# Kernel optimization log

Measured on AMD Instinct MI355X. Metric: run time of the kernel, lower is better.

## Reference

```python
import jax, jax.numpy as jnp
import numpy as np
import math

DIM = 1024
N_HEADS = 16
HEAD_DIM = DIM // N_HEADS
MAX_SEQ_LEN = 2048


def rope_tables(seq_len, head_dim):
    inv_freq = 1.0 / (10000.0 ** (jnp.arange(0, head_dim, 2, dtype=jnp.float32) / head_dim))
    t = jnp.arange(seq_len, dtype=jnp.float32)
    freqs = jnp.einsum('i,j->ij', t, inv_freq)          # [T, D/2]
    emb = jnp.concatenate([freqs, freqs], axis=-1)      # [T, D]
    return jnp.cos(emb), jnp.sin(emb)


def rotate_half(x):
    x1, x2 = jnp.split(x, 2, axis=-1)
    return jnp.concatenate([-x2, x1], axis=-1)


def setup_inputs() -> dict:
    key = jax.random.key(0)
    k1, k2, k3 = jax.random.split(key, 3)
    B, T = 4, 2048
    x = jax.random.normal(k1, (B, T, DIM), dtype=jnp.float32)
    # Linear(dim, 3*dim, bias=False) and Linear(dim, dim, bias=False); stored as [in, out]
    Wqkv = jax.random.normal(k2, (DIM, 3 * DIM), dtype=jnp.float32) * (1.0 / math.sqrt(DIM))
    Wproj = jax.random.normal(k3, (DIM, DIM), dtype=jnp.float32) * (1.0 / math.sqrt(DIM))
    return {"x": x, "Wqkv": Wqkv, "Wproj": Wproj}


def reference(x, Wqkv, Wproj):
    B, T, C = x.shape
    qkv = x @ Wqkv                                       # [B,T,3C]
    q, k, v = jnp.split(qkv, 3, axis=-1)
    # [B,T,C] -> [B,H,T,D]
    def to_heads(t_):
        return t_.reshape(B, T, N_HEADS, HEAD_DIM).transpose(0, 2, 1, 3)
    q, k, v = to_heads(q), to_heads(k), to_heads(v)
    cos, sin = rope_tables(T, HEAD_DIM)                  # [T,D]
    cos = cos[None, None, :, :]
    sin = sin[None, None, :, :]
    q = q * cos + rotate_half(q) * sin
    k = k * cos + rotate_half(k) * sin
    scale = 1.0 / math.sqrt(HEAD_DIM)
    att = jnp.einsum('bhqd,bhkd->bhqk', q, k) * scale    # [B,H,T,T]
    causal = jnp.triu(jnp.ones((T, T), dtype=bool), k=1)
    att = jnp.where(causal[None, None], -jnp.inf, att)
    att = jax.nn.softmax(att, axis=-1)
    y = jnp.einsum('bhqk,bhkd->bhqd', att, v)            # [B,H,T,D]
    y = y.transpose(0, 2, 1, 3).reshape(B, T, C)
    return y @ Wproj
```

## Files before the change

### kernel.cpp

```cpp
#include <hip/hip_runtime.h>
#include <hip/hip_bf16.h>

typedef unsigned short u16;
typedef __attribute__((ext_vector_type(8))) short short8;
typedef __attribute__((ext_vector_type(4))) float floatx4;

__device__ __forceinline__ u16 f2bf(float f) {
    union { float f; unsigned u; } v; v.f = f;
    unsigned r = v.u + 0x7fffu + ((v.u >> 16) & 1u);
    return (u16)(r >> 16);
}
__device__ __forceinline__ float fexp2(float x) {
#if __has_builtin(__builtin_amdgcn_exp2f)
    return __builtin_amdgcn_exp2f(x);
#else
    return exp2f(x);
#endif
}

__device__ __forceinline__ void async_load16(const void* g, void* l) {
    __builtin_amdgcn_global_load_lds(
        (const __attribute__((address_space(1))) unsigned int*)g,
        (__attribute__((address_space(3))) unsigned int*)l, 16, 0, 0);
}

#define B_   4
#define T_   2048
#define NH_  16
#define HD_  64
#define DIM_ 1024
#define M_   (B_ * T_)
#define NQKV (3 * DIM_)
#define LOG2E 1.4426950408889634f

__global__ void cvt_x(const float* __restrict__ in, u16* __restrict__ out) {
    int idx = blockIdx.x * 256 + threadIdx.x;
    float4 v = ((const float4*)in)[idx];
    ushort4 o;
    o.x = f2bf(v.x); o.y = f2bf(v.y); o.z = f2bf(v.z); o.w = f2bf(v.w);
    ((ushort4*)out)[idx] = o;
}

__global__ void transpose_cvt(const float* __restrict__ in, u16* __restrict__ out,
                              int R, int Cn) {
    __shared__ float tile[32][33];
    int c0 = blockIdx.x * 32, r0 = blockIdx.y * 32;
    int tx = threadIdx.x, ty = threadIdx.y;
#pragma unroll
    for (int i = 0; i < 4; ++i)
        tile[ty + i * 8][tx] = in[(size_t)(r0 + ty + i * 8) * Cn + c0 + tx];
    __syncthreads();
#pragma unroll
    for (int i = 0; i < 4; ++i)
        out[(size_t)(c0 + ty + i * 8) * R + r0 + tx] = f2bf(tile[tx][ty + i * 8]);
}

__global__ void rope_table(float* __restrict__ tabc, float* __restrict__ tabs) {
    int idx = blockIdx.x * 256 + threadIdx.x;
    if (idx >= T_ * 32) return;
    int t = idx >> 5, j = idx & 31;
    double invf = pow(10000.0, -(double)j / 32.0);
    double th = (double)t * invf;
    tabc[idx] = (float)cos(th);
    tabs[idx] = (float)sin(th);
}

__global__ void v_transpose(const u16* __restrict__ Vh, u16* __restrict__ Vt) {
    __shared__ u16 tile[64 * 68];
    const int tid = threadIdx.x;
    const int bh = blockIdx.y, b = bh >> 4, h = bh & 15;
    const int t0 = blockIdx.x * 64;
    {
        int lr = tid >> 2;
        int lc = tid & 3;
        const u16* src = Vh + ((size_t)(b * T_ + t0 + lr)) * DIM_ + h * HD_;
#pragma unroll
        for (int j = 0; j < 4; ++j) {
            int c = (lc + j * 4) * 4;
            *(uint2*)&tile[lr * 68 + c] = *(const uint2*)(src + c);
        }
    }
    __syncthreads();
    {
        int d2 = tid >> 3, tseg = tid & 7;
        u16 lo8[8], hi8[8];
#pragma unroll
        for (int j = 0; j < 8; ++j) {
            unsigned w = *(const unsigned*)&tile[(tseg * 8 + j) * 68 + d2 * 2];
            lo8[j] = (u16)(w & 0xffffu);
            hi8[j] = (u16)(w >> 16);
        }
        size_t ob = ((size_t)bh * HD_ + 2 * d2) * T_ + t0 + tseg * 8;
        *(uint4*)(Vt + ob) = *(const uint4*)lo8;
        *(uint4*)(Vt + ob + T_) = *(const uint4*)hi8;
    }
}

__global__ __launch_bounds__(256) void gemm_qkv(const u16* __restrict__ A,
                                                const u16* __restrict__ Bt,
                                                const float* __restrict__ tabc,
                                                const float* __restrict__ tabs,
                                                u16* __restrict__ Qo,
                                                u16* __restrict__ Ko,
                                                u16* __restrict__ Vh) {
    __shared__ __align__(16) u16 smem[2 * 128 * 64];
    u16* Asl = smem;
    u16* Bsl = smem + 128 * 64;
    const int tid = threadIdx.x;
    const int wave = tid >> 6, lane = tid & 63;
    const int ln15 = lane & 15, quad = lane >> 4;
    const int m0 = blockIdx.y * 128, n0 = blockIdx.x * 128;
    const int wm = (wave & 1) * 64, wn = (wave >> 1) * 64;
    const int l8 = lane & 7, ld8 = lane >> 3;
    const int sgc = (l8 ^ ld8) * 8;
    const int K = DIM_;

    floatx4 acc[4][4] = {};

    for (int k0 = 0; k0 < K; k0 += 64) {
#pragma unroll
        for (int it = 0; it < 4; ++it) {
            int rb = wave * 32 + it * 8;
            async_load16(A  + (size_t)(m0 + rb + ld8) * K + k0 + sgc, &Asl[rb * 64]);
            async_load16(Bt + (size_t)(n0 + rb + ld8) * K + k0 + sgc, &Bsl[rb * 64]);
        }
        __syncthreads();
#pragma unroll
        for (int kk = 0; kk < 64; kk += 32) {
            const int c4 = kk >> 3;
            short8 af[4], bfm[4];
#pragma unroll
            for (int i = 0; i < 4; ++i) {
                int row = wm + i * 16 + ln15;
                af[i] = *(const short8*)&Asl[row * 64 + (((c4 + quad) ^ (row & 7)) << 3)];
            }
#pragma unroll
            for (int jj = 0; jj < 4; ++jj) {
                int row = wn + jj * 16 + ln15;
                bfm[jj] = *(const short8*)&Bsl[row * 64 + (((c4 + quad) ^ (row & 7)) << 3)];
            }
#pragma unroll
            for (int i = 0; i < 4; ++i)
#pragma unroll
                for (int jj = 0; jj < 4; ++jj)
                    acc[i][jj] = __builtin_amdgcn_mfma_f32_16x16x32_bf16(
                        af[i], bfm[jj], acc[i][jj], 0, 0, 0);
        }
        __syncthreads();
    }

    u16* Es = smem;
    const int sel = n0 >> 10;
    auto es_put = [&](int row, int col, u16 v) {
        int c = col >> 3;
        int pc = (c & 8) | ((c & 7) ^ (row & 7));
        Es[row * 128 + pc * 8 + (col & 7)] = v;
    };
    if (sel == 2) {
#pragma unroll
        for (int i = 0; i < 4; ++i)
#pragma unroll
            for (int jj = 0; jj < 4; ++jj)
#pragma unroll
                for (int r = 0; r < 4; ++r)
                    es_put(wm + i * 16 + quad * 4 + r, wn + jj * 16 + ln15,
                           f2bf(acc[i][jj][r]));
    } else {
        const float scale = sel ? 1.0f : 0.125f * LOG2E;
#pragma unroll
        for (int i = 0; i < 4; ++i)
#pragma unroll
            for (int jjl = 0; jjl < 2; ++jjl) {
                int j = jjl * 16 + ln15;
#pragma unroll
                for (int r = 0; r < 4; ++r) {
                    int row = wm + i * 16 + quad * 4 + r;
                    int t = (m0 + row) & (T_ - 1);
                    float cs = tabc[t * 32 + j], sn = tabs[t * 32 + j];
                    float xl = acc[i][jjl][r], xh = acc[i][jjl + 2][r];
                    es_put(row, wn + j,      f2bf((xl * cs - xh * sn) * scale));
                    es_put(row, wn + j + 32, f2bf((xh * cs + xl * sn) * scale));
                }
            }
    }
    __syncthreads();
    const int bb = m0 >> 11;
    u16* outqk = (sel == 1) ? Ko : Qo;
#pragma unroll
    for (int k = 0; k < 8; ++k) {
        int cid = tid + k * 256;
        int row = cid >> 4, c = cid & 15;
        int pc = (c & 8) | ((c & 7) ^ (row & 7));
        uint4 v = *(const uint4*)&Es[row * 128 + pc * 8];
        if (sel == 2) {
            *(uint4*)&Vh[(size_t)(m0 + row) * DIM_ + (n0 & 1023) + c * 8] = v;
        } else {
            int h = ((n0 & 1023) >> 6) + (c >> 3);
            int d = (c & 7) * 8;
            int t = (m0 + row) & (T_ - 1);
            *(uint4*)&outqk[((size_t)(bb * NH_ + h) * T_ + t) * HD_ + d] = v;
        }
    }
}

__global__ __launch_bounds__(256) void gemm_bt_f32(const u16* __restrict__ A,
                                                   const u16* __restrict__ Bt,
                                                   float* __restrict__ C,
                                                   int M, int N, int K) {
    __shared__ __align__(16) u16 Asl[128 * 64];
    __shared__ __align__(16) u16 Bsl[128 * 64];
    const int tid = threadIdx.x;
    const int wave = tid >> 6, lane = tid & 63;
    const int ln15 = lane & 15, quad = lane >> 4;
    const int m0 = blockIdx.y * 128, n0 = blockIdx.x * 128;
    const int wm = (wave & 1) * 64, wn = (wave >> 1) * 64;
    const int l8 = lane & 7, ld8 = lane >> 3;
    const int sgc = (l8 ^ ld8) * 8;

    floatx4 acc[4][4] = {};

    for (int k0 = 0; k0 < K; k0 += 64) {
#pragma unroll
        for (int it = 0; it < 4; ++it) {
            int rb = wave * 32 + it * 8;
            async_load16(A  + (size_t)(m0 + rb + ld8) * K + k0 + sgc, &Asl[rb * 64]);
            async_load16(Bt + (size_t)(n0 + rb + ld8) * K + k0 + sgc, &Bsl[rb * 64]);
        }
        __syncthreads();
#pragma unroll
        for (int kk = 0; kk < 64; kk += 32) {
            const int c4 = kk >> 3;
            short8 af[4], bfm[4];
#pragma unroll
            for (int i = 0; i < 4; ++i) {
                int row = wm + i * 16 + ln15;
                af[i] = *(const short8*)&Asl[row * 64 + (((c4 + quad) ^ (row & 7)) << 3)];
            }
#pragma unroll
            for (int jj = 0; jj < 4; ++jj) {
                int row = wn + jj * 16 + ln15;
                bfm[jj] = *(const short8*)&Bsl[row * 64 + (((c4 + quad) ^ (row & 7)) << 3)];
            }
#pragma unroll
            for (int i = 0; i < 4; ++i)
#pragma unroll
                for (int jj = 0; jj < 4; ++jj)
                    acc[i][jj] = __builtin_amdgcn_mfma_f32_16x16x32_bf16(
                        af[i], bfm[jj], acc[i][jj], 0, 0, 0);
        }
        __syncthreads();
    }
#pragma unroll
    for (int i = 0; i < 4; ++i)
#pragma unroll
        for (int jj = 0; jj < 4; ++jj)
#pragma unroll
            for (int r = 0; r < 4; ++r) {
                int m = m0 + wm + i * 16 + quad * 4 + r;
                int n = n0 + wn + jj * 16 + ln15;
                C[(size_t)m * N + n] = acc[i][jj][r];
            }
}

__global__ __launch_bounds__(256, 4) void attn_kernel(const u16* __restrict__ Q,
                                                      const u16* __restrict__ Kh,
                                                      const u16* __restrict__ Vt,
                                                      u16* __restrict__ Y) {
    __shared__ __align__(16) u16 Kl[2][64 * 64];
    __shared__ __align__(16) u16 Vl[2][64 * 64];
    __shared__ __align__(16) u16 Pl[4][16 * 64];
    const int tid = threadIdx.x, wave = tid >> 6, lane = tid & 63;
    const int ln15 = lane & 15, quad = lane >> 4;
    const int p = blockIdx.x;
    const int bh = blockIdx.y;
    const int b = bh >> 4, h = bh & 15;
    const int l8 = lane & 7, ld8 = lane >> 3;
    const int sgc = l8 ^ ld8;

    const u16* kbase = Kh + (size_t)bh * T_ * HD_;
    const u16* vbase = Vt + (size_t)bh * HD_ * T_;
    const short8 ones = {0x3F80, 0x3F80, 0x3F80, 0x3F80,
                         0x3F80, 0x3F80, 0x3F80, 0x3F80};
    const int srow = wave * 16;

#pragma unroll
    for (int half = 0; half < 2; ++half) {
        const int tidx = half ? p : (31 - p);
        const int q0 = tidx * 64;
        const int bm = q0 + srow;

        const u16* qp = Q + ((size_t)bh * T_ + bm + ln15) * HD_;
        short8 qf0 = *(const short8*)(qp + quad * 8);
        short8 qf1 = *(const short8*)(qp + 32 + quad * 8);

        floatx4 o[5] = {};

        __syncthreads();
#pragma unroll
        for (int it = 0; it < 2; ++it) {
            int r = srow + it * 8;
            async_load16(kbase + (size_t)(r + ld8) * HD_ + sgc * 8, &Kl[0][r * 64]);
            async_load16(vbase + (size_t)(r + ld8) * T_ + sgc * 8, &Vl[0][r * 64]);
        }

        for (int kt = 0; kt <= tidx; ++kt) {
            const int cur = kt & 1;
            __syncthreads();
            if (kt < tidx) {
                const int kn = (kt + 1) * 64;
#pragma unroll
                for (int it = 0; it < 2; ++it) {
                    int r = srow + it * 8;
                    async_load16(kbase + (size_t)(kn + r + ld8) * HD_ + sgc * 8,
                                 &Kl[cur ^ 1][r * 64]);
                    async_load16(vbase + (size_t)(r + ld8) * T_ + kn + sgc * 8,
                                 &Vl[cur ^ 1][r * 64]);
                }
            }
            floatx4 s[4] = {};
#pragma unroll
            for (int nt = 0; nt < 4; ++nt) {
                int row = nt * 16 + ln15;
                short8 kf0 = *(const short8*)&Kl[cur][row * 64 + ((quad ^ (row & 7)) << 3)];
                short8 kf1 = *(const short8*)&Kl[cur][row * 64 + (((4 + quad) ^ (row & 7)) << 3)];
                s[nt] = __builtin_amdgcn_mfma_f32_16x16x32_bf16(qf0, kf0, s[nt], 0, 0, 0);
                s[nt] = __builtin_amdgcn_mfma_f32_16x16x32_bf16(qf1, kf1, s[nt], 0, 0, 0);
            }
            if (kt == tidx) {
#pragma unroll
                for (int nt = 0; nt < 4; ++nt) {
                    int key = nt * 16 + ln15, lim = srow + quad * 4;
#pragma unroll
                    for (int r = 0; r < 4; ++r)
                        s[nt][r] = (key > lim + r) ? 0.f : fexp2(s[nt][r]);
                }
            } else {
#pragma unroll
                for (int nt = 0; nt < 4; ++nt)
#pragma unroll
                    for (int r = 0; r < 4; ++r) s[nt][r] = fexp2(s[nt][r]);
            }
            u16* pw = Pl[wave];
#pragma unroll
            for (int nt = 0; nt < 4; ++nt) {
                int kc = nt * 2 + (ln15 >> 3), k7 = ln15 & 7;
#pragma unroll
                for (int r = 0; r < 4; ++r) {
                    int row = quad * 4 + r;
                    pw[row * 64 + ((kc ^ (row & 7)) << 3) + k7] = f2bf(s[nt][r]);
                }
            }
            short8 pf0 = *(const short8*)&pw[ln15 * 64 + ((quad ^ (ln15 & 7)) << 3)];
            short8 pf1 = *(const short8*)&pw[ln15 * 64 + (((4 + quad) ^ (ln15 & 7)) << 3)];
#pragma unroll
            for (int nt = 0; nt < 4; ++nt) {
                int row = nt * 16 + ln15;
                short8 vf0 = *(const short8*)&Vl[cur][row * 64 + ((quad ^ (row & 7)) << 3)];
                short8 vf1 = *(const short8*)&Vl[cur][row * 64 + (((4 + quad) ^ (row & 7)) << 3)];
                o[nt] = __builtin_amdgcn_mfma_f32_16x16x32_bf16(pf0, vf0, o[nt], 0, 0, 0);
                o[nt] = __builtin_amdgcn_mfma_f32_16x16x32_bf16(pf1, vf1, o[nt], 0, 0, 0);
            }
            o[4] = __builtin_amdgcn_mfma_f32_16x16x32_bf16(pf0, ones, o[4], 0, 0, 0);
            o[4] = __builtin_amdgcn_mfma_f32_16x16x32_bf16(pf1, ones, o[4], 0, 0, 0);
        }
#pragma unroll
        for (int r = 0; r < 4; ++r) {
            float inv = 1.f / o[4][r];
            int row = bm + quad * 4 + r;
            u16* yp = Y + ((size_t)(b * T_ + row)) * DIM_ + h * HD_;
#pragma unroll
            for (int nt = 0; nt < 4; ++nt)
                yp[nt * 16 + ln15] = f2bf(o[nt][r] * inv);
        }
    }
}

extern "C" void kernel_launch(void* const* d_in, const int* in_sizes, int n_in,
                              void* d_out, int out_size, void* d_ws, size_t ws_size,
                              hipStream_t stream) {
    const float* x     = (const float*)d_in[0];
    const float* Wqkv  = (const float*)d_in[1];
    const float* Wproj = (const float*)d_in[2];
    float* out = (float*)d_out;
    char* ws = (char*)d_ws;

    const size_t SZ_XB  = (size_t)M_ * DIM_ * 2;
    const size_t SZ_WQT = (size_t)NQKV * DIM_ * 2;
    const size_t SZ_WPT = (size_t)DIM_ * DIM_ * 2;
    const size_t SZ_Q   = SZ_XB;
    const size_t SZ_TAB = (size_t)T_ * 32 * 4;

    u16*   xb   = (u16*)(ws);
    u16*   wqt  = (u16*)(ws + SZ_XB);
    u16*   wpt  = (u16*)(ws + SZ_XB + SZ_WQT);
    u16*   qb   = (u16*)(ws + SZ_XB + SZ_WQT + SZ_WPT);
    u16*   kb   = (u16*)(ws + SZ_XB + SZ_WQT + SZ_WPT + SZ_Q);
    u16*   vhb  = (u16*)(ws + SZ_XB + SZ_WQT + SZ_WPT + 2 * SZ_Q);
    u16*   vtb  = (u16*)(ws + SZ_XB + SZ_WQT + SZ_WPT + 3 * SZ_Q);
    float* tabc = (float*)(ws + SZ_XB + SZ_WQT + SZ_WPT + 4 * SZ_Q);
    float* tabs = (float*)(ws + SZ_XB + SZ_WQT + SZ_WPT + 4 * SZ_Q + SZ_TAB);
    u16*   yb   = xb;

    rope_table<<<(T_ * 32 + 255) / 256, 256, 0, stream>>>(tabc, tabs);
    cvt_x<<<(M_ * DIM_ / 4) / 256, 256, 0, stream>>>(x, xb);
    transpose_cvt<<<dim3(NQKV / 32, DIM_ / 32), dim3(32, 8), 0, stream>>>(Wqkv, wqt, DIM_, NQKV);
    transpose_cvt<<<dim3(DIM_ / 32, DIM_ / 32), dim3(32, 8), 0, stream>>>(Wproj, wpt, DIM_, DIM_);
    gemm_qkv<<<dim3(NQKV / 128, M_ / 128), 256, 16384, stream>>>(xb, wqt, tabc, tabs, qb, kb, vhb);
    v_transpose<<<dim3(T_ / 64, B_ * NH_), 256, 0, stream>>>(vhb, vtb);
    attn_kernel<<<dim3(16, B_ * NH_), 256, 0, stream>>>(qb, kb, vtb, yb);
    gemm_bt_f32<<<dim3(DIM_ / 128, M_ / 128), 256, 0, stream>>>(yb, wpt, out, M_, DIM_, DIM_);
}
```

Measured before the change: 268.2 us.

## Rebuild QKV and projection GEMMs with triple-buffered async pipeline and larger tiles

Both bf16 GEMMs move to a shared core that uses 512-thread blocks computing 128x256 tiles. Global-to-LDS loads are triple-buffered and issued two k-steps ahead, with explicit vmcnt waits and split barriers so loads overlap MFMA work. MFMA sections are bracketed by setprio, and block IDs are remapped so neighbouring blocks share operands in cache. The QKV epilogue staging is widened to 256 columns. The cost is 144KB of LDS per block, which limits occupancy and leaves the projection GEMM with only 256 blocks.

```diff
diff --git a/kernel.cpp b/kernel.cpp
--- a/kernel.cpp
+++ b/kernel.cpp
@@ -31,6 +31,7 @@
 #define DIM_ 1024
 #define M_   (B_ * T_)
 #define NQKV (3 * DIM_)
+#define NT_  16
 #define LOG2E 1.4426950408889634f
 
 __global__ void cvt_x(const float* __restrict__ in, u16* __restrict__ out) {
@@ -96,75 +97,122 @@
     }
 }
 
-__global__ __launch_bounds__(256) void gemm_qkv(const u16* __restrict__ A,
-                                                const u16* __restrict__ Bt,
-                                                const float* __restrict__ tabc,
-                                                const float* __restrict__ tabs,
-                                                u16* __restrict__ Qo,
-                                                u16* __restrict__ Ko,
-                                                u16* __restrict__ Vh) {
-    __shared__ __align__(16) u16 smem[2 * 128 * 64];
-    u16* Asl = smem;
-    u16* Bsl = smem + 128 * 64;
-    const int tid = threadIdx.x;
+__device__ __forceinline__ void gemm_core(const u16* __restrict__ A,
+                                          const u16* __restrict__ Bt,
+                                          u16* smem, int m0, int n0, int tid,
+                                          floatx4 (&acc)[4][4]) {
     const int wave = tid >> 6, lane = tid & 63;
     const int ln15 = lane & 15, quad = lane >> 4;
-    const int m0 = blockIdx.y * 128, n0 = blockIdx.x * 128;
     const int wm = (wave & 1) * 64, wn = (wave >> 1) * 64;
     const int l8 = lane & 7, ld8 = lane >> 3;
     const int sgc = (l8 ^ ld8) * 8;
     const int K = DIM_;
 
+    const u16* aS = A + (size_t)(m0 + wave * 16 + ld8) * K + sgc;
+    const u16* bS = Bt + (size_t)(n0 + wave * 32 + ld8) * K + sgc;
+
+    auto issueA_B0 = [&](int k2, u16* As2, u16* Bs2) {
+        async_load16(aS + k2,          As2 + (wave * 16) * 64);
+        async_load16(aS + 8 * K + k2,  As2 + (wave * 16 + 8) * 64);
+        async_load16(bS + k2,          Bs2 + (wave * 32) * 64);
+    };
+    auto issueB123 = [&](int k2, u16* Bs2) {
+        async_load16(bS + 8 * K + k2,  Bs2 + (wave * 32 + 8) * 64);
+        async_load16(bS + 16 * K + k2, Bs2 + (wave * 32 + 16) * 64);
+        async_load16(bS + 24 * K + k2, Bs2 + (wave * 32 + 24) * 64);
+    };
+    auto compute = [&](const u16* As_c, const u16* Bs_c, int c4) {
+        short8 af[4], bfv[4];
+#pragma unroll
+        for (int i = 0; i < 4; ++i) {
+            int row = wm + i * 16 + ln15;
+            af[i] = *(const short8*)&As_c[row * 64 + (((c4 + quad) ^ (row & 7)) << 3)];
+        }
+#pragma unroll
+        for (int j = 0; j < 4; ++j) {
+            int row = wn + j * 16 + ln15;
+            bfv[j] = *(const short8*)&Bs_c[row * 64 + (((c4 + quad) ^ (row & 7)) << 3)];
+        }
+        __builtin_amdgcn_s_setprio(1);
+#pragma unroll
+        for (int i = 0; i < 4; ++i)
+#pragma unroll
+            for (int j = 0; j < 4; ++j)
+                acc[i][j] = __builtin_amdgcn_mfma_f32_16x16x32_bf16(
+                    af[i], bfv[j], acc[i][j], 0, 0, 0);
+        __builtin_amdgcn_s_setprio(0);
+    };
+
+    issueA_B0(0, smem, smem + 24576);
+    issueB123(0, smem + 24576);
+    issueA_B0(64, smem + 8192, smem + 24576 + 16384);
+    issueB123(64, smem + 24576 + 16384);
+
+#pragma unroll 1
+    for (int t = 0; t < NT_; ++t) {
+        if (t < NT_ - 1) asm volatile("s_waitcnt vmcnt(6)" ::: "memory");
+        else             asm volatile("s_waitcnt vmcnt(0)" ::: "memory");
+        __builtin_amdgcn_s_barrier();
+        asm volatile("" ::: "memory");
+
+        const int cb = t % 3, cb2 = (t + 2) % 3;
+        const u16* As_c = smem + cb * 8192;
+        const u16* Bs_c = smem + 24576 + cb * 16384;
+        u16* As2 = smem + cb2 * 8192;
+        u16* Bs2 = smem + 24576 + cb2 * 16384;
+        const bool iss = t < NT_ - 2;
+        const int k2 = (t + 2) * 64;
+
+        if (iss) issueA_B0(k2, As2, Bs2);
+        compute(As_c, Bs_c, 0);
+        asm volatile("" ::: "memory");
+        __builtin_amdgcn_s_barrier();
+        asm volatile("" ::: "memory");
+
+        if (iss) issueB123(k2, Bs2);
+        compute(As_c, Bs_c, 4);
+        asm volatile("" ::: "memory");
+    }
+}
+
+__global__ __launch_bounds__(512, 2) void gemm_qkv(const u16* __restrict__ A,
+                                                   const u16* __restrict__ Bt,
+                                                   const float* __restrict__ tabc,
+                                                   const float* __restrict__ tabs,
+                                                   u16* __restrict__ Qo,
+                                                   u16* __restrict__ Ko,
+                                                   u16* __restrict__ Vh) {
+    __shared__ __align__(16) u16 smem[73728];
+    const int tid = threadIdx.x;
+    const int bid = blockIdx.x;
+    const int wg = (bid & 7) * 96 + (bid >> 3);
+    const int bx = wg / 64, by = wg - bx * 64;
+    const int m0 = by * 128, n0 = bx * 256;
+
     floatx4 acc[4][4] = {};
-
-    for (int k0 = 0; k0 < K; k0 += 64) {
-#pragma unroll
-        for (int it = 0; it < 4; ++it) {
-            int rb = wave * 32 + it * 8;
-            async_load16(A  + (size_t)(m0 + rb + ld8) * K + k0 + sgc, &Asl[rb * 64]);
-            async_load16(Bt + (size_t)(n0 + rb + ld8) * K + k0 + sgc, &Bsl[rb * 64]);
-        }
-        __syncthreads();
-#pragma unroll
-        for (int kk = 0; kk < 64; kk += 32) {
-            const int c4 = kk >> 3;
-            short8 af[4], bfm[4];
-#pragma unroll
-            for (int i = 0; i < 4; ++i) {
-                int row = wm + i * 16 + ln15;
-                af[i] = *(const short8*)&Asl[row * 64 + (((c4 + quad) ^ (row & 7)) << 3)];
-            }
-#pragma unroll
-            for (int jj = 0; jj < 4; ++jj) {
-                int row = wn + jj * 16 + ln15;
-                bfm[jj] = *(const short8*)&Bsl[row * 64 + (((c4 + quad) ^ (row & 7)) << 3)];
-            }
-#pragma unroll
-            for (int i = 0; i < 4; ++i)
-#pragma unroll
-                for (int jj = 0; jj < 4; ++jj)
-                    acc[i][jj] = __builtin_amdgcn_mfma_f32_16x16x32_bf16(
-                        af[i], bfm[jj], acc[i][jj], 0, 0, 0);
-        }
-        __syncthreads();
-    }
-
+    gemm_core(A, Bt, smem, m0, n0, tid, acc);
+
+    const int wave = tid >> 6, lane = tid & 63;
+    const int ln15 = lane & 15, quad = lane >> 4;
+    const int wm = (wave & 1) * 64, wn = (wave >> 1) * 64;
+
+    __syncthreads();
     u16* Es = smem;
     const int sel = n0 >> 10;
     auto es_put = [&](int row, int col, u16 v) {
         int c = col >> 3;
-        int pc = (c & 8) | ((c & 7) ^ (row & 7));
-        Es[row * 128 + pc * 8 + (col & 7)] = v;
+        int pc = (c & 24) | ((c & 7) ^ (row & 7));
+        Es[row * 256 + pc * 8 + (col & 7)] = v;
     };
     if (sel == 2) {
 #pragma unroll
         for (int i = 0; i < 4; ++i)
 #pragma unroll
-            for (int jj = 0; jj < 4; ++jj)
+            for (int j = 0; j < 4; ++j)
 #pragma unroll
                 for (int r = 0; r < 4; ++r)
-                    es_put(wm + i * 16 + quad * 4 + r, wn + jj * 16 + ln15,
-                           f2bf(acc[i][jj][r]));
+                    es_put(wm + i * 16 + quad * 4 + r, wn + j * 16 + ln15,
+                           f2bf(acc[i][j][r]));
     } else {
         const float scale = sel ? 1.0f : 0.125f * LOG2E;
 #pragma unroll
@@ -188,10 +236,10 @@
     u16* outqk = (sel == 1) ? Ko : Qo;
 #pragma unroll
     for (int k = 0; k < 8; ++k) {
-        int cid = tid + k * 256;
-        int row = cid >> 4, c = cid & 15;
-        int pc = (c & 8) | ((c & 7) ^ (row & 7));
-        uint4 v = *(const uint4*)&Es[row * 128 + pc * 8];
+        int cid = tid + k * 512;
+        int row = cid >> 5, c = cid & 31;
+        int pc = (c & 24) | ((c & 7) ^ (row & 7));
+        uint4 v = *(const uint4*)&Es[row * 256 + pc * 8];
         if (sel == 2) {
             *(uint4*)&Vh[(size_t)(m0 + row) * DIM_ + (n0 & 1023) + c * 8] = v;
         } else {
@@ -203,62 +251,31 @@
     }
 }
 
-__global__ __launch_bounds__(256) void gemm_bt_f32(const u16* __restrict__ A,
-                                                   const u16* __restrict__ Bt,
-                                                   float* __restrict__ C,
-                                                   int M, int N, int K) {
-    __shared__ __align__(16) u16 Asl[128 * 64];
-    __shared__ __align__(16) u16 Bsl[128 * 64];
+__global__ __launch_bounds__(512, 2) void gemm_proj(const u16* __restrict__ A,
+                                                    const u16* __restrict__ Bt,
+                                                    float* __restrict__ C) {
+    __shared__ __align__(16) u16 smem[73728];
     const int tid = threadIdx.x;
+    const int bid = blockIdx.x;
+    const int wg = (bid & 7) * 32 + (bid >> 3);
+    const int bx = wg / 64, by = wg - bx * 64;
+    const int m0 = by * 128, n0 = bx * 256;
+
+    floatx4 acc[4][4] = {};
+    gemm_core(A, Bt, smem, m0, n0, tid, acc);
+
     const int wave = tid >> 6, lane = tid & 63;
     const int ln15 = lane & 15, quad = lane >> 4;
-    const int m0 = blockIdx.y * 128, n0 = blockIdx.x * 128;
     const int wm = (wave & 1) * 64, wn = (wave >> 1) * 64;
-    const int l8 = lane & 7, ld8 = lane >> 3;
-    const int sgc = (l8 ^ ld8) * 8;
-
-    floatx4 acc[4][4] = {};
-
-    for (int k0 = 0; k0 < K; k0 += 64) {
-#pragma unroll
-        for (int it = 0; it < 4; ++it) {
-            int rb = wave * 32 + it * 8;
-            async_load16(A  + (size_t)(m0 + rb + ld8) * K + k0 + sgc, &Asl[rb * 64]);
-            async_load16(Bt + (size_t)(n0 + rb + ld8) * K + k0 + sgc, &Bsl[rb * 64]);
-        }
-        __syncthreads();
-#pragma unroll
-        for (int kk = 0; kk < 64; kk += 32) {
-            const int c4 = kk >> 3;
-            short8 af[4], bfm[4];
-#pragma unroll
-            for (int i = 0; i < 4; ++i) {
-                int row = wm + i * 16 + ln15;
-                af[i] = *(const short8*)&Asl[row * 64 + (((c4 + quad) ^ (row & 7)) << 3)];
-            }
-#pragma unroll
-            for (int jj = 0; jj < 4; ++jj) {
-                int row = wn + jj * 16 + ln15;
-                bfm[jj] = *(const short8*)&Bsl[row * 64 + (((c4 + quad) ^ (row & 7)) << 3)];
-            }
-#pragma unroll
-            for (int i = 0; i < 4; ++i)
-#pragma unroll
-                for (int jj = 0; jj < 4; ++jj)
-                    acc[i][jj] = __builtin_amdgcn_mfma_f32_16x16x32_bf16(
-                        af[i], bfm[jj], acc[i][jj], 0, 0, 0);
-        }
-        __syncthreads();
-    }
 #pragma unroll
     for (int i = 0; i < 4; ++i)
 #pragma unroll
-        for (int jj = 0; jj < 4; ++jj)
+        for (int j = 0; j < 4; ++j)
 #pragma unroll
             for (int r = 0; r < 4; ++r) {
                 int m = m0 + wm + i * 16 + quad * 4 + r;
-                int n = n0 + wn + jj * 16 + ln15;
-                C[(size_t)m * N + n] = acc[i][jj][r];
+                int n = n0 + wn + j * 16 + ln15;
+                C[(size_t)m * DIM_ + n] = acc[i][j][r];
             }
 }
 
@@ -405,8 +422,8 @@
     cvt_x<<<(M_ * DIM_ / 4) / 256, 256, 0, stream>>>(x, xb);
     transpose_cvt<<<dim3(NQKV / 32, DIM_ / 32), dim3(32, 8), 0, stream>>>(Wqkv, wqt, DIM_, NQKV);
     transpose_cvt<<<dim3(DIM_ / 32, DIM_ / 32), dim3(32, 8), 0, stream>>>(Wproj, wpt, DIM_, DIM_);
-    gemm_qkv<<<dim3(NQKV / 128, M_ / 128), 256, 16384, stream>>>(xb, wqt, tabc, tabs, qb, kb, vhb);
+    gemm_qkv<<<768, 512, 0, stream>>>(xb, wqt, tabc, tabs, qb, kb, vhb);
     v_transpose<<<dim3(T_ / 64, B_ * NH_), 256, 0, stream>>>(vhb, vtb);
     attn_kernel<<<dim3(16, B_ * NH_), 256, 0, stream>>>(qb, kb, vtb, yb);
-    gemm_bt_f32<<<dim3(DIM_ / 128, M_ / 128), 256, 0, stream>>>(yb, wpt, out, M_, DIM_, DIM_);
-}
+    gemm_proj<<<256, 512, 0, stream>>>(yb, wpt, out);
+}
```

Measured after the change: 262.8 us. 1.02x faster.
